# Kernel optimization log

Hardware: AMD Instinct MI355X
Metric: run time of the kernel (lower is better)

## Reference

```python
import jax, jax.numpy as jnp
import numpy as np

B, S, D = 16, 1024, 384
H, DH = 6, 64  # head_dim = hidden // heads


def setup_inputs() -> dict:
    key = jax.random.key(0)
    ks = jax.random.split(key, 9)
    std = 0.02
    return {
        "x": jax.random.normal(ks[0], (B, S, D), jnp.float32),
        "Wq": jax.random.normal(ks[1], (H, D, DH), jnp.float32) * std,
        "bq": jax.random.normal(ks[2], (H, DH), jnp.float32) * std,
        "Wk": jax.random.normal(ks[3], (H, D, DH), jnp.float32) * std,
        "bk": jax.random.normal(ks[4], (H, DH), jnp.float32) * std,
        "Wv": jax.random.normal(ks[5], (H, D, DH), jnp.float32) * std,
        "bv": jax.random.normal(ks[6], (H, DH), jnp.float32) * std,
        "Wo": jax.random.normal(ks[7], (D, D), jnp.float32) * std,  # [out, in] like nn.Linear
        "bo": jax.random.normal(ks[8], (D,), jnp.float32) * std,
    }


def reference(x, Wq, bq, Wk, bk, Wv, bv, Wo, bo):
    # Per-head q/k/v projections (stacked over heads h)
    q = jnp.einsum("bsd,hde->bhse", x, Wq) + bq[None, :, None, :]
    k = jnp.einsum("bsd,hde->bhse", x, Wk) + bk[None, :, None, :]
    v = jnp.einsum("bsd,hde->bhse", x, Wv) + bv[None, :, None, :]
    # Explicit softmax attention (dropout prob = 0.0 in config)
    scores = jnp.einsum("bhse,bhte->bhst", q, k) / jnp.sqrt(jnp.float32(DH))
    probs = jax.nn.softmax(scores, axis=-1)
    ctx = jnp.einsum("bhst,bhte->bhse", probs, v)  # [B,H,S,DH]
    # Concat heads along last dim: [B,S,H*DH]
    concat = jnp.transpose(ctx, (0, 2, 1, 3)).reshape(B, S, H * DH)
    # Output projection (nn.Linear: y = x @ W^T + b)
    out = jnp.einsum("bsd,ed->bse", concat, Wo) + bo
    return out
```

## Files before the change

### kernel.cpp

```cpp
#include <hip/hip_runtime.h>
#include <hip/hip_bf16.h>

typedef __attribute__((ext_vector_type(8))) short short8;
typedef __attribute__((ext_vector_type(4))) short short4v;
typedef __attribute__((ext_vector_type(4))) float float4v;

#define MFMA16(a,b,c) __builtin_amdgcn_mfma_f32_16x16x32_bf16((a),(b),(c),0,0,0)
#define EXP2(x) __builtin_amdgcn_exp2f(x)

static constexpr int Bz = 16, Sq = 1024, Dm = 384, Hh = 6, Dh = 64;
static constexpr int Mtok = Bz * Sq;
static constexpr int NQKV = 1152;

__device__ __forceinline__ short f2bf(float f) {
  union { float f; unsigned u; } v; v.f = f;
  unsigned r = v.u + 0x7fffu + ((v.u >> 16) & 1u);
  return (short)(r >> 16);
}

__device__ __forceinline__ void gload16(const void* src, void* lds) {
  __builtin_amdgcn_global_load_lds(
      (const __attribute__((address_space(1))) unsigned int*)src,
      (__attribute__((address_space(3))) unsigned int*)lds, 16, 0, 0);
}

__global__ __launch_bounds__(256) void conv_x(const float* __restrict__ x,
                                              short* __restrict__ xb) {
  const int i = (blockIdx.x * 256 + threadIdx.x) * 8;
  float4v v0 = *(const float4v*)(x + i);
  float4v v1 = *(const float4v*)(x + i + 4);
  short8 o;
  o[0] = f2bf(v0[0]); o[1] = f2bf(v0[1]); o[2] = f2bf(v0[2]); o[3] = f2bf(v0[3]);
  o[4] = f2bf(v1[0]); o[5] = f2bf(v1[1]); o[6] = f2bf(v1[2]); o[7] = f2bf(v1[3]);
  *(short8*)(xb + i) = o;
}

__global__ __launch_bounds__(256) void conv_w(const float* __restrict__ Wq,
                                              const float* __restrict__ Wk,
                                              const float* __restrict__ Wv,
                                              const float* __restrict__ bq,
                                              const float* __restrict__ bk,
                                              const float* __restrict__ bv,
                                              const float* __restrict__ Wo,
                                              short* __restrict__ Wt,
                                              float* __restrict__ bias,
                                              short* __restrict__ Wob) {
  const float SCL = 0.125f * 1.44269504088896340736f;
  const int i = blockIdx.x * 256 + threadIdx.x;
  const int NW = NQKV * Dm;
  if (i < NW) {
    const int c = i / Dm, d = i % Dm;
    const int p = c / 384, rr = c % 384;
    const int h = rr >> 6, dh = rr & 63;
    const float* W = (p == 0) ? Wq : ((p == 1) ? Wk : Wv);
    float w = W[(h * Dm + d) * Dh + dh];
    if (p == 0) w *= SCL;
    Wt[c * Dm + d] = f2bf(w);
  } else if (i < NW + NQKV) {
    const int c = i - NW;
    const int p = c / 384, rr = c % 384;
    const int h = rr >> 6, dh = rr & 63;
    const float* bb = (p == 0) ? bq : ((p == 1) ? bk : bv);
    float b = bb[h * Dh + dh];
    if (p == 0) b *= SCL;
    bias[c] = b;
  } else if (i < NW + NQKV + Dm * Dm) {
    const int j = i - NW - NQKV;
    Wob[j] = f2bf(Wo[j]);
  }
}


__global__ __launch_bounds__(256) void qkv_gemm(const short* __restrict__ Xb,
                                                const short* __restrict__ Wt,
                                                const float* __restrict__ bias,
                                                short* __restrict__ qkv,
                                                short* __restrict__ vt) {
  __shared__ char smem[32768];
  const int tid = threadIdx.x;
  const int wave = tid >> 6, lane = tid & 63;
  const int r = lane & 15, g = lane >> 4;
  const int wr = wave >> 1, wc = wave & 1;

  const int flat = blockIdx.x;
  const int w = (flat & 7) * 144 + (flat >> 3);
  const int bx = w % 9, by = w / 9;
  const int bm0 = by * 128, bn0 = bx * 128;
  const int m0 = bm0 + wr * 64, n0 = bn0 + wc * 64;

  float bv_n[4];
#pragma unroll
  for (int ni = 0; ni < 4; ++ni) bv_n[ni] = bias[n0 + ni * 16 + r];
  asm volatile("s_waitcnt vmcnt(0)" ::: "memory");

  const char *aSrc0, *aSrc1, *bSrc0, *bSrc1;
  {
    const int o0 = tid * 16, o1 = 4096 + tid * 16;
    const int lr0 = o0 >> 7, cb0 = (o0 & 127) ^ ((lr0 & 7) << 4);
    const int lr1 = o1 >> 7, cb1 = (o1 & 127) ^ ((lr1 & 7) << 4);
    const int m_0 = 2 * lr0 + (cb0 >> 6), kb0 = cb0 & 63;
    const int m_1 = 2 * lr1 + (cb1 >> 6), kb1 = cb1 & 63;
    aSrc0 = (const char*)(Xb + (bm0 + m_0) * Dm) + kb0;
    aSrc1 = (const char*)(Xb + (bm0 + m_1) * Dm) + kb1;
    bSrc0 = (const char*)(Wt + (bn0 + m_0) * Dm) + kb0;
    bSrc1 = (const char*)(Wt + (bn0 + m_1) * Dm) + kb1;
  }
  auto stage = [&](int t, int buf) {
    char* base = smem + buf * 16384;
    const int kb = t * 64;
    gload16(aSrc0 + kb, base + wave * 1024);
    gload16(aSrc1 + kb, base + 4096 + wave * 1024);
    gload16(bSrc0 + kb, base + 8192 + wave * 1024);
    gload16(bSrc1 + kb, base + 12288 + wave * 1024);
  };

  int aOff[4], bOff[4];
#pragma unroll
  for (int i = 0; i < 4; ++i) {
    const int m = wr * 64 + i * 16 + r;
    const int lr = m >> 1;
    aOff[i] = lr * 128 + ((((m & 1) << 6) | (16 * g)) ^ ((lr & 7) << 4));
    const int n = wc * 64 + i * 16 + r;
    const int lrn = n >> 1;
    bOff[i] = 8192 + lrn * 128 + ((((n & 1) << 6) | (16 * g)) ^ ((lrn & 7) << 4));
  }

  float4v acc[4][4] = {};
  auto compute = [&](int buf) {
    const char* sb = smem + buf * 16384;
    short8 a[4], b[4];
#pragma unroll
    for (int i = 0; i < 4; ++i) a[i] = *(const short8*)(sb + aOff[i]);
#pragma unroll
    for (int i = 0; i < 4; ++i) b[i] = *(const short8*)(sb + bOff[i]);
#pragma unroll
    for (int mi = 0; mi < 4; ++mi)
#pragma unroll
      for (int ni = 0; ni < 4; ++ni)
        acc[mi][ni] = MFMA16(a[mi], b[ni], acc[mi][ni]);
  };

  stage(0, 0);
  stage(1, 1);
  for (int t = 0; t < 11; ++t) {
    asm volatile("s_waitcnt vmcnt(4)" ::: "memory");
    __builtin_amdgcn_s_barrier();
    compute(t & 1);
    __builtin_amdgcn_s_barrier();
    if (t < 10) stage(t + 2, t & 1);
  }
  asm volatile("s_waitcnt vmcnt(0)" ::: "memory");
  __builtin_amdgcn_s_barrier();
  compute(1);

#pragma unroll
  for (int ni = 0; ni < 4; ++ni) {
    const int col = n0 + ni * 16 + r;
    const int p = col / 384, rr2 = col % 384;
    const int h = rr2 >> 6, dh = rr2 & 63;
    const float bv = bv_n[ni];
#pragma unroll
    for (int mi = 0; mi < 4; ++mi) {
#pragma unroll
      for (int reg = 0; reg < 4; ++reg) {
        const int mg = m0 + mi * 16 + 4 * g + reg;
        const short o = f2bf(acc[mi][ni][reg] + bv);
        if (p < 2) {
          qkv[mg * NQKV + col] = o;
        } else {
          const int bb = mg >> 10, s = mg & 1023;
          vt[((bb * Hh + h) * Dh + dh) * Sq + s] = o;
        }
      }
    }
  }
}

__global__ __launch_bounds__(256) void attn(const short* __restrict__ qkv,
                                            const short* __restrict__ vt,
                                            short* __restrict__ ctx) {
  __shared__ char smem[32768];
  const int tid = threadIdx.x;
  const int wave = tid >> 6, lane = tid & 63;
  const int r = lane & 15, g = lane >> 4;
  const int xr = (r & 7) << 4;
  const int flat = blockIdx.x;
  const int w = (flat & 7) * 96 + (flat >> 3);
  const int qb = w & 7, bh = w >> 3;
  const int b = bh / Hh, h = bh % Hh;
  const int tok0 = b * Sq;
  const int qw = qb * 128 + wave * 32;

  short8 qf[2][2];
#pragma unroll
  for (int f = 0; f < 2; ++f) {
    const short* qp = qkv + (tok0 + qw + 16 * f + r) * NQKV + h * Dh;
    qf[f][0] = *(const short8*)(qp + 8 * g);
    qf[f][1] = *(const short8*)(qp + 32 + 8 * g);
  }
  asm volatile("s_waitcnt vmcnt(0)" ::: "memory");

  const short* kg = qkv + tok0 * NQKV + 384 + h * Dh;
  const short* vg = vt + (b * Hh + h) * Dh * Sq;

  const int o0 = wave * 2048 + lane * 16;
  const int row0 = o0 >> 7, cb0 = (o0 & 127) ^ ((row0 & 7) << 4);
  const int o1 = o0 + 1024;
  const int row1 = o1 >> 7, cb1 = (o1 & 127) ^ ((row1 & 7) << 4);

#define STAGE(T, BUFSEL)                                                        \
  {                                                                             \
    char* kb_ = smem + (BUFSEL) * 16384;                                        \
    const int kv_ = (T) * 64;                                                   \
    gload16((const char*)(kg + (kv_ + row0) * NQKV) + cb0, kb_ + wave * 2048);  \
    gload16((const char*)(vg + row0 * Sq + kv_) + cb0, kb_ + 8192 + wave * 2048);\
    gload16((const char*)(kg + (kv_ + row1) * NQKV) + cb1, kb_ + wave * 2048 + 1024);\
    gload16((const char*)(vg + row1 * Sq + kv_) + cb1, kb_ + 8192 + wave * 2048 + 1024);\
  }

  int kOff[4][2], vOff[4][2];
#pragma unroll
  for (int kt = 0; kt < 4; ++kt)
#pragma unroll
    for (int c = 0; c < 2; ++c)
      kOff[kt][c] = (16 * kt + r) * 128 + ((64 * c + 16 * g) ^ xr);
#pragma unroll
  for (int d = 0; d < 4; ++d)
#pragma unroll
    for (int h2 = 0; h2 < 2; ++h2)
      vOff[d][h2] = (16 * d + r) * 128 + ((64 * h2 + 8 * g) ^ xr);

  float4v acc[4][2] = {};
  float lsum[2] = {0.f, 0.f};

  auto compute = [&](int bufsel) {
    const char* kb = smem + bufsel * 16384;
    const char* vb = kb + 8192;
    short8 kf[4][2];
#pragma unroll
    for (int kt = 0; kt < 4; ++kt) {
      kf[kt][0] = *(const short8*)(kb + kOff[kt][0]);
      kf[kt][1] = *(const short8*)(kb + kOff[kt][1]);
    }
    short8 vf[4][2];
#pragma unroll
    for (int d = 0; d < 4; ++d)
#pragma unroll
      for (int h2 = 0; h2 < 2; ++h2) {
        short4v lo = *(const short4v*)(vb + vOff[d][h2]);
        short4v hi = *(const short4v*)(vb + (vOff[d][h2] ^ 32));
        short8 t;
        t[0] = lo[0]; t[1] = lo[1]; t[2] = lo[2]; t[3] = lo[3];
        t[4] = hi[0]; t[5] = hi[1]; t[6] = hi[2]; t[7] = hi[3];
        vf[d][h2] = t;
      }
    float4v s[4][2];
#pragma unroll
    for (int kt = 0; kt < 4; ++kt)
#pragma unroll
      for (int f = 0; f < 2; ++f) {
        float4v z = {};
        z = MFMA16(kf[kt][0], qf[f][0], z);
        z = MFMA16(kf[kt][1], qf[f][1], z);
        s[kt][f] = z;
      }
    short8 pa[2][2];
#pragma unroll
    for (int f = 0; f < 2; ++f) {
      float ps = 0.f;
#pragma unroll
      for (int h2 = 0; h2 < 2; ++h2) {
#pragma unroll
        for (int j = 0; j < 4; ++j) {
          const float e0 = EXP2(s[2 * h2][f][j]);
          const float e1 = EXP2(s[2 * h2 + 1][f][j]);
          pa[f][h2][j]     = f2bf(e0);
          pa[f][h2][4 + j] = f2bf(e1);
          ps += e0 + e1;
        }
      }
      lsum[f] += ps;
    }
#pragma unroll
    for (int d = 0; d < 4; ++d)
#pragma unroll
      for (int f = 0; f < 2; ++f) {
        acc[d][f] = MFMA16(pa[f][0], vf[d][0], acc[d][f]);
        acc[d][f] = MFMA16(pa[f][1], vf[d][1], acc[d][f]);
      }
  };

  STAGE(0, 0)
  STAGE(1, 1)
  for (int t = 0; t < 15; ++t) {
    asm volatile("s_waitcnt vmcnt(4)" ::: "memory");
    __builtin_amdgcn_s_barrier();
    compute(t & 1);
    __builtin_amdgcn_s_barrier();
    if (t < 14) STAGE(t + 2, t & 1)
  }
  asm volatile("s_waitcnt vmcnt(0)" ::: "memory");
  __builtin_amdgcn_s_barrier();
  compute(1);

#pragma unroll
  for (int f = 0; f < 2; ++f) {
    lsum[f] += __shfl_xor(lsum[f], 16);
    lsum[f] += __shfl_xor(lsum[f], 32);
  }
#pragma unroll
  for (int f = 0; f < 2; ++f) {
    float il[4];
#pragma unroll
    for (int reg = 0; reg < 4; ++reg) il[reg] = 1.f / __shfl(lsum[f], 4 * g + reg);
#pragma unroll
    for (int d = 0; d < 4; ++d) {
      short* cp = ctx + (tok0 + qw + 16 * f + 4 * g) * Dm + h * Dh + 16 * d + r;
#pragma unroll
      for (int reg = 0; reg < 4; ++reg)
        cp[reg * Dm] = f2bf(acc[d][f][reg] * il[reg]);
    }
  }
}

__global__ __launch_bounds__(256) void out_gemm(const short* __restrict__ ctx,
                                                const short* __restrict__ Wob,
                                                const float* __restrict__ bo,
                                                float* __restrict__ out) {
  __shared__ char smem[32768];
  const int tid = threadIdx.x;
  const int wave = tid >> 6, lane = tid & 63;
  const int r = lane & 15, g = lane >> 4;
  const int wr = wave >> 1, wc = wave & 1;

  const int flat = blockIdx.x;
  const int w = (flat & 7) * 48 + (flat >> 3);
  const int bx = w % 3, by = w / 3;
  const int bm0 = by * 128, bn0 = bx * 128;
  const int m0 = bm0 + wr * 64, n0 = bn0 + wc * 64;

  float bv_n[4];
#pragma unroll
  for (int ni = 0; ni < 4; ++ni) bv_n[ni] = bo[n0 + ni * 16 + r];
  asm volatile("s_waitcnt vmcnt(0)" ::: "memory");

  const char *aSrc0, *aSrc1, *bSrc0, *bSrc1;
  {
    const int o0 = tid * 16, o1 = 4096 + tid * 16;
    const int lr0 = o0 >> 7, cb0 = (o0 & 127) ^ ((lr0 & 7) << 4);
    const int lr1 = o1 >> 7, cb1 = (o1 & 127) ^ ((lr1 & 7) << 4);
    const int m_0 = 2 * lr0 + (cb0 >> 6), kb0 = cb0 & 63;
    const int m_1 = 2 * lr1 + (cb1 >> 6), kb1 = cb1 & 63;
    aSrc0 = (const char*)(ctx + (bm0 + m_0) * Dm) + kb0;
    aSrc1 = (const char*)(ctx + (bm0 + m_1) * Dm) + kb1;
    bSrc0 = (const char*)(Wob + (bn0 + m_0) * Dm) + kb0;
    bSrc1 = (const char*)(Wob + (bn0 + m_1) * Dm) + kb1;
  }
  auto stage = [&](int t, int buf) {
    char* base = smem + buf * 16384;
    const int kb = t * 64;
    gload16(aSrc0 + kb, base + wave * 1024);
    gload16(aSrc1 + kb, base + 4096 + wave * 1024);
    gload16(bSrc0 + kb, base + 8192 + wave * 1024);
    gload16(bSrc1 + kb, base + 12288 + wave * 1024);
  };

  int aOff[4], bOff[4];
#pragma unroll
  for (int i = 0; i < 4; ++i) {
    const int m = wr * 64 + i * 16 + r;
    const int lr = m >> 1;
    aOff[i] = lr * 128 + ((((m & 1) << 6) | (16 * g)) ^ ((lr & 7) << 4));
    const int n = wc * 64 + i * 16 + r;
    const int lrn = n >> 1;
    bOff[i] = 8192 + lrn * 128 + ((((n & 1) << 6) | (16 * g)) ^ ((lrn & 7) << 4));
  }

  float4v acc[4][4] = {};
  auto compute = [&](int buf) {
    const char* sb = smem + buf * 16384;
    short8 a[4], b[4];
#pragma unroll
    for (int i = 0; i < 4; ++i) a[i] = *(const short8*)(sb + aOff[i]);
#pragma unroll
    for (int i = 0; i < 4; ++i) b[i] = *(const short8*)(sb + bOff[i]);
#pragma unroll
    for (int mi = 0; mi < 4; ++mi)
#pragma unroll
      for (int ni = 0; ni < 4; ++ni)
        acc[mi][ni] = MFMA16(a[mi], b[ni], acc[mi][ni]);
  };

  stage(0, 0);
  stage(1, 1);
  for (int t = 0; t < 11; ++t) {
    asm volatile("s_waitcnt vmcnt(4)" ::: "memory");
    __builtin_amdgcn_s_barrier();
    compute(t & 1);
    __builtin_amdgcn_s_barrier();
    if (t < 10) stage(t + 2, t & 1);
  }
  asm volatile("s_waitcnt vmcnt(0)" ::: "memory");
  __builtin_amdgcn_s_barrier();
  compute(1);

#pragma unroll
  for (int ni = 0; ni < 4; ++ni) {
    const int col = n0 + ni * 16 + r;
    const float bv = bv_n[ni];
#pragma unroll
    for (int mi = 0; mi < 4; ++mi) {
#pragma unroll
      for (int reg = 0; reg < 4; ++reg) {
        const int mg = m0 + mi * 16 + 4 * g + reg;
        out[mg * Dm + col] = acc[mi][ni][reg] + bv;
      }
    }
  }
}

extern "C" void kernel_launch(void* const* d_in, const int* in_sizes, int n_in,
                              void* d_out, int out_size, void* d_ws, size_t ws_size,
                              hipStream_t stream) {
  const float* x  = (const float*)d_in[0];
  const float* Wq = (const float*)d_in[1];
  const float* bq = (const float*)d_in[2];
  const float* Wk = (const float*)d_in[3];
  const float* bk = (const float*)d_in[4];
  const float* Wv = (const float*)d_in[5];
  const float* bv = (const float*)d_in[6];
  const float* Wo = (const float*)d_in[7];
  const float* bo = (const float*)d_in[8];
  float* out = (float*)d_out;

  char* ws = (char*)d_ws;
  short* Xb   = (short*)(ws);
  short* Wt   = (short*)(ws + 12582912);
  float* bias = (float*)(ws + 13467648);
  short* Wob  = (short*)(ws + 13472256);
  short* qkv  = (short*)(ws + 13767168);
  short* vt   = (short*)(ws + 51515904);
  short* ctx  = (short*)(ws + 64098816);

  conv_x<<<Mtok * Dm / (256 * 8), 256, 0, stream>>>(x, Xb);
  conv_w<<<(NQKV * Dm + NQKV + Dm * Dm + 255) / 256, 256, 0, stream>>>(
      Wq, Wk, Wv, bq, bk, bv, Wo, Wt, bias, Wob);
  qkv_gemm<<<1152, 256, 0, stream>>>(Xb, Wt, bias, qkv, vt);
  attn<<<768, 256, 0, stream>>>(qkv, vt, ctx);
  out_gemm<<<384, 256, 0, stream>>>(ctx, Wob, bo, out);
}
```

Baseline: 114.2 us.

## Double the K-step per pipeline stage in GEMMs and attention KV tiles

All three kernels now stage twice as much data per pipeline step: the GEMMs load 64-element K chunks (128 bytes per row) instead of 32, and attention loads 128 keys per step instead of 64. Shared memory per block doubles to 64 KB, and the loop trip counts halve, which cuts the number of barriers and wait points per tile. The LDS swizzle layout is reworked to a plain row-major XOR pattern, and attention's inner loop is restructured to interleave QK, exp and PV per 32-key chunk. The cost is more LDS per block, which may lower occupancy, and more outstanding loads in flight.

```diff
diff --git a/kernel.cpp b/kernel.cpp
--- a/kernel.cpp
+++ b/kernel.cpp
@@ -76,10 +76,11 @@
                                                 const float* __restrict__ bias,
                                                 short* __restrict__ qkv,
                                                 short* __restrict__ vt) {
-  __shared__ char smem[32768];
+  __shared__ char smem[65536];
   const int tid = threadIdx.x;
   const int wave = tid >> 6, lane = tid & 63;
   const int r = lane & 15, g = lane >> 4;
+  const int xr = (r & 7) << 4;
   const int wr = wave >> 1, wc = wave & 1;
 
   const int flat = blockIdx.x;
@@ -93,61 +94,64 @@
   for (int ni = 0; ni < 4; ++ni) bv_n[ni] = bias[n0 + ni * 16 + r];
   asm volatile("s_waitcnt vmcnt(0)" ::: "memory");
 
-  const char *aSrc0, *aSrc1, *bSrc0, *bSrc1;
-  {
-    const int o0 = tid * 16, o1 = 4096 + tid * 16;
-    const int lr0 = o0 >> 7, cb0 = (o0 & 127) ^ ((lr0 & 7) << 4);
-    const int lr1 = o1 >> 7, cb1 = (o1 & 127) ^ ((lr1 & 7) << 4);
-    const int m_0 = 2 * lr0 + (cb0 >> 6), kb0 = cb0 & 63;
-    const int m_1 = 2 * lr1 + (cb1 >> 6), kb1 = cb1 & 63;
-    aSrc0 = (const char*)(Xb + (bm0 + m_0) * Dm) + kb0;
-    aSrc1 = (const char*)(Xb + (bm0 + m_1) * Dm) + kb1;
-    bSrc0 = (const char*)(Wt + (bn0 + m_0) * Dm) + kb0;
-    bSrc1 = (const char*)(Wt + (bn0 + m_1) * Dm) + kb1;
+  const char *aS[4], *bS[4];
+#pragma unroll
+  for (int j = 0; j < 4; ++j) {
+    const int o = j * 4096 + tid * 16;
+    const int lr = o >> 7;
+    const int cb = (o & 127) ^ ((lr & 7) << 4);
+    aS[j] = (const char*)(Xb + (bm0 + lr) * Dm) + cb;
+    bS[j] = (const char*)(Wt + (bn0 + lr) * Dm) + cb;
   }
   auto stage = [&](int t, int buf) {
-    char* base = smem + buf * 16384;
-    const int kb = t * 64;
-    gload16(aSrc0 + kb, base + wave * 1024);
-    gload16(aSrc1 + kb, base + 4096 + wave * 1024);
-    gload16(bSrc0 + kb, base + 8192 + wave * 1024);
-    gload16(bSrc1 + kb, base + 12288 + wave * 1024);
-  };
-
-  int aOff[4], bOff[4];
-#pragma unroll
-  for (int i = 0; i < 4; ++i) {
-    const int m = wr * 64 + i * 16 + r;
-    const int lr = m >> 1;
-    aOff[i] = lr * 128 + ((((m & 1) << 6) | (16 * g)) ^ ((lr & 7) << 4));
-    const int n = wc * 64 + i * 16 + r;
-    const int lrn = n >> 1;
-    bOff[i] = 8192 + lrn * 128 + ((((n & 1) << 6) | (16 * g)) ^ ((lrn & 7) << 4));
-  }
+    char* base = smem + buf * 32768;
+#pragma unroll
+    for (int j = 0; j < 4; ++j) {
+      gload16(aS[j] + t * 128, base + j * 4096 + tid * 16);
+      gload16(bS[j] + t * 128, base + 16384 + j * 4096 + tid * 16);
+    }
+  };
+
+  int aOff[4][2], bOff[4][2];
+#pragma unroll
+  for (int i = 0; i < 4; ++i)
+#pragma unroll
+    for (int c = 0; c < 2; ++c) {
+      aOff[i][c] = (wr * 64 + i * 16 + r) * 128 + ((64 * c + 16 * g) ^ xr);
+      bOff[i][c] = 16384 + (wc * 64 + i * 16 + r) * 128 + ((64 * c + 16 * g) ^ xr);
+    }
 
   float4v acc[4][4] = {};
   auto compute = [&](int buf) {
-    const char* sb = smem + buf * 16384;
-    short8 a[4], b[4];
-#pragma unroll
-    for (int i = 0; i < 4; ++i) a[i] = *(const short8*)(sb + aOff[i]);
-#pragma unroll
-    for (int i = 0; i < 4; ++i) b[i] = *(const short8*)(sb + bOff[i]);
+    const char* sb = smem + buf * 32768;
+    short8 a[4][2], b[4][2];
+#pragma unroll
+    for (int i = 0; i < 4; ++i) {
+      a[i][0] = *(const short8*)(sb + aOff[i][0]);
+      a[i][1] = *(const short8*)(sb + aOff[i][1]);
+    }
+#pragma unroll
+    for (int i = 0; i < 4; ++i) {
+      b[i][0] = *(const short8*)(sb + bOff[i][0]);
+      b[i][1] = *(const short8*)(sb + bOff[i][1]);
+    }
 #pragma unroll
     for (int mi = 0; mi < 4; ++mi)
 #pragma unroll
-      for (int ni = 0; ni < 4; ++ni)
-        acc[mi][ni] = MFMA16(a[mi], b[ni], acc[mi][ni]);
+      for (int ni = 0; ni < 4; ++ni) {
+        acc[mi][ni] = MFMA16(a[mi][0], b[ni][0], acc[mi][ni]);
+        acc[mi][ni] = MFMA16(a[mi][1], b[ni][1], acc[mi][ni]);
+      }
   };
 
   stage(0, 0);
   stage(1, 1);
-  for (int t = 0; t < 11; ++t) {
-    asm volatile("s_waitcnt vmcnt(4)" ::: "memory");
+  for (int t = 0; t < 5; ++t) {
+    asm volatile("s_waitcnt vmcnt(8)" ::: "memory");
     __builtin_amdgcn_s_barrier();
     compute(t & 1);
     __builtin_amdgcn_s_barrier();
-    if (t < 10) stage(t + 2, t & 1);
+    if (t < 4) stage(t + 2, t & 1);
   }
   asm volatile("s_waitcnt vmcnt(0)" ::: "memory");
   __builtin_amdgcn_s_barrier();
@@ -179,7 +183,7 @@
 __global__ __launch_bounds__(256) void attn(const short* __restrict__ qkv,
                                             const short* __restrict__ vt,
                                             short* __restrict__ ctx) {
-  __shared__ char smem[32768];
+  __shared__ char smem[65536];
   const int tid = threadIdx.x;
   const int wave = tid >> 6, lane = tid & 63;
   const int r = lane & 15, g = lane >> 4;
@@ -203,101 +207,97 @@
   const short* kg = qkv + tok0 * NQKV + 384 + h * Dh;
   const short* vg = vt + (b * Hh + h) * Dh * Sq;
 
-  const int o0 = wave * 2048 + lane * 16;
-  const int row0 = o0 >> 7, cb0 = (o0 & 127) ^ ((row0 & 7) << 4);
-  const int o1 = o0 + 1024;
-  const int row1 = o1 >> 7, cb1 = (o1 & 127) ^ ((row1 & 7) << 4);
-
-#define STAGE(T, BUFSEL)                                                        \
-  {                                                                             \
-    char* kb_ = smem + (BUFSEL) * 16384;                                        \
-    const int kv_ = (T) * 64;                                                   \
-    gload16((const char*)(kg + (kv_ + row0) * NQKV) + cb0, kb_ + wave * 2048);  \
-    gload16((const char*)(vg + row0 * Sq + kv_) + cb0, kb_ + 8192 + wave * 2048);\
-    gload16((const char*)(kg + (kv_ + row1) * NQKV) + cb1, kb_ + wave * 2048 + 1024);\
-    gload16((const char*)(vg + row1 * Sq + kv_) + cb1, kb_ + 8192 + wave * 2048 + 1024);\
-  }
-
-  int kOff[4][2], vOff[4][2];
-#pragma unroll
-  for (int kt = 0; kt < 4; ++kt)
+  const char *kS[4], *vS[4];
+#pragma unroll
+  for (int j = 0; j < 4; ++j) {
+    const int o = j * 4096 + tid * 16;
+    const int kr = o >> 7;
+    const int kcb = (o & 127) ^ ((kr & 7) << 4);
+    kS[j] = (const char*)(kg + kr * NQKV) + kcb;
+    const int vr = o >> 8;
+    const int vcb = (o & 255) ^ ((vr & 7) << 4);
+    vS[j] = (const char*)(vg + vr * Sq) + vcb;
+  }
+  auto stage = [&](int t, int buf) {
+    char* base = smem + buf * 32768;
+    const size_t krow = (size_t)t * 128 * NQKV * 2;
+#pragma unroll
+    for (int j = 0; j < 4; ++j) {
+      gload16(kS[j] + krow, base + j * 4096 + tid * 16);
+      gload16(vS[j] + t * 256, base + 16384 + j * 4096 + tid * 16);
+    }
+  };
+
+  int kOff[8][2], vOff[4][4];
+#pragma unroll
+  for (int kt = 0; kt < 8; ++kt)
 #pragma unroll
     for (int c = 0; c < 2; ++c)
       kOff[kt][c] = (16 * kt + r) * 128 + ((64 * c + 16 * g) ^ xr);
 #pragma unroll
   for (int d = 0; d < 4; ++d)
 #pragma unroll
-    for (int h2 = 0; h2 < 2; ++h2)
-      vOff[d][h2] = (16 * d + r) * 128 + ((64 * h2 + 8 * g) ^ xr);
+    for (int kk = 0; kk < 4; ++kk)
+      vOff[d][kk] = 16384 + (16 * d + r) * 256 + ((kk * 64 + 8 * g) ^ xr);
 
   float4v acc[4][2] = {};
   float lsum[2] = {0.f, 0.f};
 
-  auto compute = [&](int bufsel) {
-    const char* kb = smem + bufsel * 16384;
-    const char* vb = kb + 8192;
-    short8 kf[4][2];
-#pragma unroll
-    for (int kt = 0; kt < 4; ++kt) {
-      kf[kt][0] = *(const short8*)(kb + kOff[kt][0]);
-      kf[kt][1] = *(const short8*)(kb + kOff[kt][1]);
-    }
-    short8 vf[4][2];
-#pragma unroll
-    for (int d = 0; d < 4; ++d)
-#pragma unroll
-      for (int h2 = 0; h2 < 2; ++h2) {
-        short4v lo = *(const short4v*)(vb + vOff[d][h2]);
-        short4v hi = *(const short4v*)(vb + (vOff[d][h2] ^ 32));
-        short8 t;
-        t[0] = lo[0]; t[1] = lo[1]; t[2] = lo[2]; t[3] = lo[3];
-        t[4] = hi[0]; t[5] = hi[1]; t[6] = hi[2]; t[7] = hi[3];
-        vf[d][h2] = t;
-      }
-    float4v s[4][2];
-#pragma unroll
-    for (int kt = 0; kt < 4; ++kt)
+  auto compute = [&](int buf) {
+    const char* kb = smem + buf * 32768;
+#pragma unroll
+    for (int kk = 0; kk < 4; ++kk) {
+      short8 kf0[2], kf1[2];
+#pragma unroll
+      for (int c = 0; c < 2; ++c) {
+        kf0[c] = *(const short8*)(kb + kOff[2 * kk][c]);
+        kf1[c] = *(const short8*)(kb + kOff[2 * kk + 1][c]);
+      }
+      float4v s0[2], s1[2];
 #pragma unroll
       for (int f = 0; f < 2; ++f) {
-        float4v z = {};
-        z = MFMA16(kf[kt][0], qf[f][0], z);
-        z = MFMA16(kf[kt][1], qf[f][1], z);
-        s[kt][f] = z;
-      }
-    short8 pa[2][2];
-#pragma unroll
-    for (int f = 0; f < 2; ++f) {
-      float ps = 0.f;
-#pragma unroll
-      for (int h2 = 0; h2 < 2; ++h2) {
+        float4v z0 = {}, z1 = {};
+        z0 = MFMA16(kf0[0], qf[f][0], z0);
+        z0 = MFMA16(kf0[1], qf[f][1], z0);
+        z1 = MFMA16(kf1[0], qf[f][0], z1);
+        z1 = MFMA16(kf1[1], qf[f][1], z1);
+        s0[f] = z0; s1[f] = z1;
+      }
+      short8 pa[2];
+#pragma unroll
+      for (int f = 0; f < 2; ++f) {
+        float ps = 0.f;
 #pragma unroll
         for (int j = 0; j < 4; ++j) {
-          const float e0 = EXP2(s[2 * h2][f][j]);
-          const float e1 = EXP2(s[2 * h2 + 1][f][j]);
-          pa[f][h2][j]     = f2bf(e0);
-          pa[f][h2][4 + j] = f2bf(e1);
+          const float e0 = EXP2(s0[f][j]);
+          const float e1 = EXP2(s1[f][j]);
+          pa[f][j]     = f2bf(e0);
+          pa[f][4 + j] = f2bf(e1);
           ps += e0 + e1;
         }
-      }
-      lsum[f] += ps;
-    }
-#pragma unroll
-    for (int d = 0; d < 4; ++d)
-#pragma unroll
-      for (int f = 0; f < 2; ++f) {
-        acc[d][f] = MFMA16(pa[f][0], vf[d][0], acc[d][f]);
-        acc[d][f] = MFMA16(pa[f][1], vf[d][1], acc[d][f]);
-      }
-  };
-
-  STAGE(0, 0)
-  STAGE(1, 1)
-  for (int t = 0; t < 15; ++t) {
-    asm volatile("s_waitcnt vmcnt(4)" ::: "memory");
+        lsum[f] += ps;
+      }
+#pragma unroll
+      for (int d = 0; d < 4; ++d) {
+        short4v lo = *(const short4v*)(kb + vOff[d][kk]);
+        short4v hi = *(const short4v*)(kb + (vOff[d][kk] ^ 32));
+        short8 vf;
+        vf[0]=lo[0]; vf[1]=lo[1]; vf[2]=lo[2]; vf[3]=lo[3];
+        vf[4]=hi[0]; vf[5]=hi[1]; vf[6]=hi[2]; vf[7]=hi[3];
+        acc[d][0] = MFMA16(pa[0], vf, acc[d][0]);
+        acc[d][1] = MFMA16(pa[1], vf, acc[d][1]);
+      }
+    }
+  };
+
+  stage(0, 0);
+  stage(1, 1);
+  for (int t = 0; t < 7; ++t) {
+    asm volatile("s_waitcnt vmcnt(8)" ::: "memory");
     __builtin_amdgcn_s_barrier();
     compute(t & 1);
     __builtin_amdgcn_s_barrier();
-    if (t < 14) STAGE(t + 2, t & 1)
+    if (t < 6) stage(t + 2, t & 1);
   }
   asm volatile("s_waitcnt vmcnt(0)" ::: "memory");
   __builtin_amdgcn_s_barrier();
@@ -327,10 +327,11 @@
                                                 const short* __restrict__ Wob,
                                                 const float* __restrict__ bo,
                                                 float* __restrict__ out) {
-  __shared__ char smem[32768];
+  __shared__ char smem[65536];
   const int tid = threadIdx.x;
   const int wave = tid >> 6, lane = tid & 63;
   const int r = lane & 15, g = lane >> 4;
+  const int xr = (r & 7) << 4;
   const int wr = wave >> 1, wc = wave & 1;
 
   const int flat = blockIdx.x;
@@ -344,61 +345,64 @@
   for (int ni = 0; ni < 4; ++ni) bv_n[ni] = bo[n0 + ni * 16 + r];
   asm volatile("s_waitcnt vmcnt(0)" ::: "memory");
 
-  const char *aSrc0, *aSrc1, *bSrc0, *bSrc1;
-  {
-    const int o0 = tid * 16, o1 = 4096 + tid * 16;
-    const int lr0 = o0 >> 7, cb0 = (o0 & 127) ^ ((lr0 & 7) << 4);
-    const int lr1 = o1 >> 7, cb1 = (o1 & 127) ^ ((lr1 & 7) << 4);
-    const int m_0 = 2 * lr0 + (cb0 >> 6), kb0 = cb0 & 63;
-    const int m_1 = 2 * lr1 + (cb1 >> 6), kb1 = cb1 & 63;
-    aSrc0 = (const char*)(ctx + (bm0 + m_0) * Dm) + kb0;
-    aSrc1 = (const char*)(ctx + (bm0 + m_1) * Dm) + kb1;
-    bSrc0 = (const char*)(Wob + (bn0 + m_0) * Dm) + kb0;
-    bSrc1 = (const char*)(Wob + (bn0 + m_1) * Dm) + kb1;
+  const char *aS[4], *bS[4];
+#pragma unroll
+  for (int j = 0; j < 4; ++j) {
+    const int o = j * 4096 + tid * 16;
+    const int lr = o >> 7;
+    const int cb = (o & 127) ^ ((lr & 7) << 4);
+    aS[j] = (const char*)(ctx + (bm0 + lr) * Dm) + cb;
+    bS[j] = (const char*)(Wob + (bn0 + lr) * Dm) + cb;
   }
   auto stage = [&](int t, int buf) {
-    char* base = smem + buf * 16384;
-    const int kb = t * 64;
-    gload16(aSrc0 + kb, base + wave * 1024);
-    gload16(aSrc1 + kb, base + 4096 + wave * 1024);
-    gload16(bSrc0 + kb, base + 8192 + wave * 1024);
-    gload16(bSrc1 + kb, base + 12288 + wave * 1024);
-  };
-
-  int aOff[4], bOff[4];
-#pragma unroll
-  for (int i = 0; i < 4; ++i) {
-    const int m = wr * 64 + i * 16 + r;
-    const int lr = m >> 1;
-    aOff[i] = lr * 128 + ((((m & 1) << 6) | (16 * g)) ^ ((lr & 7) << 4));
-    const int n = wc * 64 + i * 16 + r;
-    const int lrn = n >> 1;
-    bOff[i] = 8192 + lrn * 128 + ((((n & 1) << 6) | (16 * g)) ^ ((lrn & 7) << 4));
-  }
+    char* base = smem + buf * 32768;
+#pragma unroll
+    for (int j = 0; j < 4; ++j) {
+      gload16(aS[j] + t * 128, base + j * 4096 + tid * 16);
+      gload16(bS[j] + t * 128, base + 16384 + j * 4096 + tid * 16);
+    }
+  };
+
+  int aOff[4][2], bOff[4][2];
+#pragma unroll
+  for (int i = 0; i < 4; ++i)
+#pragma unroll
+    for (int c = 0; c < 2; ++c) {
+      aOff[i][c] = (wr * 64 + i * 16 + r) * 128 + ((64 * c + 16 * g) ^ xr);
+      bOff[i][c] = 16384 + (wc * 64 + i * 16 + r) * 128 + ((64 * c + 16 * g) ^ xr);
+    }
 
   float4v acc[4][4] = {};
   auto compute = [&](int buf) {
-    const char* sb = smem + buf * 16384;
-    short8 a[4], b[4];
-#pragma unroll
-    for (int i = 0; i < 4; ++i) a[i] = *(const short8*)(sb + aOff[i]);
-#pragma unroll
-    for (int i = 0; i < 4; ++i) b[i] = *(const short8*)(sb + bOff[i]);
+    const char* sb = smem + buf * 32768;
+    short8 a[4][2], b[4][2];
+#pragma unroll
+    for (int i = 0; i < 4; ++i) {
+      a[i][0] = *(const short8*)(sb + aOff[i][0]);
+      a[i][1] = *(const short8*)(sb + aOff[i][1]);
+    }
+#pragma unroll
+    for (int i = 0; i < 4; ++i) {
+      b[i][0] = *(const short8*)(sb + bOff[i][0]);
+      b[i][1] = *(const short8*)(sb + bOff[i][1]);
+    }
 #pragma unroll
     for (int mi = 0; mi < 4; ++mi)
 #pragma unroll
-      for (int ni = 0; ni < 4; ++ni)
-        acc[mi][ni] = MFMA16(a[mi], b[ni], acc[mi][ni]);
+      for (int ni = 0; ni < 4; ++ni) {
+        acc[mi][ni] = MFMA16(a[mi][0], b[ni][0], acc[mi][ni]);
+        acc[mi][ni] = MFMA16(a[mi][1], b[ni][1], acc[mi][ni]);
+      }
   };
 
   stage(0, 0);
   stage(1, 1);
-  for (int t = 0; t < 11; ++t) {
-    asm volatile("s_waitcnt vmcnt(4)" ::: "memory");
+  for (int t = 0; t < 5; ++t) {
+    asm volatile("s_waitcnt vmcnt(8)" ::: "memory");
     __builtin_amdgcn_s_barrier();
     compute(t & 1);
     __builtin_amdgcn_s_barrier();
-    if (t < 10) stage(t + 2, t & 1);
+    if (t < 4) stage(t + 2, t & 1);
   }
   asm volatile("s_waitcnt vmcnt(0)" ::: "memory");
   __builtin_amdgcn_s_barrier();
```

Result: slower. 125.6 us (+10.0%).
